# Kernel tuning notes

Measured on AMD Instinct MI355X. Metric: run time of the kernel, lower is better.

## Reference

```python
import jax, jax.numpy as jnp
import numpy as np

N = 10000      # nodes
E = 320000     # edges (before self-loops)
D_IN = 256
HID = 128
HEADS = 4
D_OUT = 256
SLOPE = 0.2    # PyG GATConv default negative_slope


def setup_inputs() -> dict:
    key = jax.random.key(0)
    ks = jax.random.split(key, 10)
    s = 0.05
    return {
        "x": jax.random.normal(ks[0], (N, D_IN), dtype=jnp.float32),
        "edge_index": jax.random.randint(ks[1], (2, E), 0, N),
        # layer 1: in=256 -> heads=4, out=128, concat
        "W1": jax.random.normal(ks[2], (D_IN, HEADS * HID), dtype=jnp.float32) * s,
        "a1_src": jax.random.normal(ks[3], (HEADS, HID), dtype=jnp.float32) * s,
        "a1_dst": jax.random.normal(ks[4], (HEADS, HID), dtype=jnp.float32) * s,
        "b1": jax.random.normal(ks[5], (HEADS * HID,), dtype=jnp.float32) * s,
        # layer 2: in=512 -> heads=1, out=256, no concat
        "W2": jax.random.normal(ks[6], (HEADS * HID, D_OUT), dtype=jnp.float32) * s,
        "a2_src": jax.random.normal(ks[7], (1, D_OUT), dtype=jnp.float32) * s,
        "a2_dst": jax.random.normal(ks[8], (1, D_OUT), dtype=jnp.float32) * s,
        "b2": jax.random.normal(ks[9], (D_OUT,), dtype=jnp.float32) * s,
    }


def gat_conv(x, src, dst, W, a_src, a_dst, bias, heads, out_dim, concat):
    """PyG-style GATConv (eval mode, self-loops pre-added to src/dst)."""
    n = x.shape[0]
    h = (x @ W).reshape(n, heads, out_dim)            # [N, H, F]
    # per-edge attention logits: LeakyReLU(a_src.h_src + a_dst.h_dst)
    as_n = (h * a_src).sum(-1)                         # [N, H]
    ad_n = (h * a_dst).sum(-1)                         # [N, H]
    logit = jax.nn.leaky_relu(as_n[src] + ad_n[dst], negative_slope=SLOPE)  # [E, H]
    # segment softmax over edges grouped by destination node
    logit = logit - jax.ops.segment_max(logit, dst, num_segments=n)[dst]
    ex = jnp.exp(logit)
    alpha = ex / jax.ops.segment_sum(ex, dst, num_segments=n)[dst]          # [E, H]
    # weighted scatter-aggregation of source messages
    out = jax.ops.segment_sum(h[src] * alpha[:, :, None], dst, num_segments=n)  # [N, H, F]
    out = out.reshape(n, heads * out_dim) if concat else out.mean(axis=1)
    return out + bias


def reference(x, edge_index, W1, a1_src, a1_dst, b1, W2, a2_src, a2_dst, b2):
    # add self-loops once (PyG GATConv default add_self_loops=True)
    loops = jnp.arange(N, dtype=edge_index.dtype)
    src = jnp.concatenate([edge_index[0], loops])
    dst = jnp.concatenate([edge_index[1], loops])
    h = gat_conv(x, src, dst, W1, a1_src, a1_dst, b1, HEADS, HID, True)
    h = jax.nn.elu(h)  # dropout is identity at eval
    return gat_conv(h, src, dst, W2, a2_src, a2_dst, b2, 1, D_OUT, False)
```

## Files before the change

kernel.cpp:

```cpp
#include <hip/hip_runtime.h>

#define N_NODES 10000
#define E_RAW   320000
#define E_TOT   330000
#define D_IN    256
#define HID     128
#define HEADS   4
#define F1      512
#define D_OUT   256
#define SLOPE   0.2f
#define EBLOCKS 1290

typedef __attribute__((ext_vector_type(8))) short bf16x8;
typedef __attribute__((ext_vector_type(4))) float f32x4;

__device__ __forceinline__ float bf2f(ushort u) {
    return __uint_as_float(((uint)u) << 16);
}
__device__ __forceinline__ ushort f2bf(float x) {
    uint u = __float_as_uint(x);
    uint r = (u + 0x7FFFu + ((u >> 16) & 1u)) >> 16;
    return (ushort)r;
}
__device__ __forceinline__ float bfu_lo(uint u) { return __uint_as_float(u << 16); }
__device__ __forceinline__ float bfu_hi(uint u) { return __uint_as_float(u & 0xFFFF0000u); }

__device__ __forceinline__ void gload_lds16(const void* g, void* l) {
    __builtin_amdgcn_global_load_lds(
        (const __attribute__((address_space(1))) void*)g,
        (__attribute__((address_space(3))) void*)l, 16, 0, 0);
}


__global__ __launch_bounds__(256) void k_zero_all(int* __restrict__ deg,
                                                  float* __restrict__ as1,
                                                  float* __restrict__ ad1,
                                                  float* __restrict__ as2,
                                                  float* __restrict__ ad2) {
    int i = blockIdx.x * 256 + threadIdx.x;
    if (i < 4 * N_NODES) { as1[i] = 0.f; ad1[i] = 0.f; }
    if (i < N_NODES) { deg[i] = 0; as2[i] = 0.f; ad2[i] = 0.f; }
}


__global__ __launch_bounds__(256) void k_hist(const int* __restrict__ ei, int* __restrict__ deg) {
    int e = blockIdx.x * 256 + threadIdx.x;
    if (e < E_TOT) {
        int dst = (e < E_RAW) ? ei[E_RAW + e] : (e - E_RAW);
        atomicAdd(&deg[dst], 1);
    }
}


#define SCAN_CHUNK 40

__global__ __launch_bounds__(256) void k_prep(const int* __restrict__ deg,
                                              int* __restrict__ row_start,
                                              int* __restrict__ cursor,
                                              const float* __restrict__ W1,
                                              ushort* __restrict__ w1h,
                                              const float* __restrict__ W2,
                                              ushort* __restrict__ w2h,
                                              const float* __restrict__ x,
                                              ushort* __restrict__ xb) {
    int b = blockIdx.x;
    int tid = threadIdx.x;
    if (b == 0) {
        __shared__ int tots[256];
        int base = tid * SCAN_CHUNK;
        int loc[SCAN_CHUNK];
        int s = 0;
        #pragma unroll
        for (int k = 0; k < SCAN_CHUNK; k++) {
            int idx = base + k;
            int v = (idx < N_NODES) ? deg[idx] : 0;
            loc[k] = s;
            s += v;
        }
        tots[tid] = s;
        __syncthreads();
        for (int off = 1; off < 256; off <<= 1) {
            int t = (tid >= off) ? tots[tid - off] : 0;
            __syncthreads();
            tots[tid] += t;
            __syncthreads();
        }
        int excl = tots[tid] - s;
        #pragma unroll
        for (int k = 0; k < SCAN_CHUNK; k++) {
            int idx = base + k;
            if (idx < N_NODES) {
                int r = excl + loc[k];
                row_start[idx] = r;
                cursor[idx]    = r;
            }
        }
        if (tid == 255) row_start[N_NODES] = E_TOT;
    } else if (b <= 64) {
        int task = (b - 1) * 4 + (tid >> 6);
        int lane = tid & 63;
        int n = (task >> 5) * 64 + lane;
        int k0 = (task & 31) * 8;
        float v[8];
        #pragma unroll
        for (int j = 0; j < 8; j++) v[j] = W1[(size_t)(k0 + j) * F1 + n];
        uint4 u;
        u.x = (uint)f2bf(v[0]) | ((uint)f2bf(v[1]) << 16);
        u.y = (uint)f2bf(v[2]) | ((uint)f2bf(v[3]) << 16);
        u.z = (uint)f2bf(v[4]) | ((uint)f2bf(v[5]) << 16);
        u.w = (uint)f2bf(v[6]) | ((uint)f2bf(v[7]) << 16);
        *(uint4*)&w1h[(size_t)n * D_IN + k0] = u;
    } else if (b <= 128) {
        int task = (b - 65) * 4 + (tid >> 6);
        int lane = tid & 63;
        int n = (task >> 6) * 64 + lane;
        int k0 = (task & 63) * 8;
        float v[8];
        #pragma unroll
        for (int j = 0; j < 8; j++) v[j] = W2[(size_t)(k0 + j) * D_OUT + n];
        uint4 u;
        u.x = (uint)f2bf(v[0]) | ((uint)f2bf(v[1]) << 16);
        u.y = (uint)f2bf(v[2]) | ((uint)f2bf(v[3]) << 16);
        u.z = (uint)f2bf(v[4]) | ((uint)f2bf(v[5]) << 16);
        u.w = (uint)f2bf(v[6]) | ((uint)f2bf(v[7]) << 16);
        *(uint4*)&w2h[(size_t)n * F1 + k0] = u;
    } else {
        int i8 = (b - 129) * 256 + tid;
        float4 a = *(const float4*)&x[(size_t)i8 * 8];
        float4 c = *(const float4*)&x[(size_t)i8 * 8 + 4];
        uint4 u;
        u.x = (uint)f2bf(a.x) | ((uint)f2bf(a.y) << 16);
        u.y = (uint)f2bf(a.z) | ((uint)f2bf(a.w) << 16);
        u.z = (uint)f2bf(c.x) | ((uint)f2bf(c.y) << 16);
        u.w = (uint)f2bf(c.z) | ((uint)f2bf(c.w) << 16);
        *(uint4*)&xb[(size_t)i8 * 8] = u;
    }
}


__global__ __launch_bounds__(256) void k_scatter(const int* __restrict__ ei,
                                                 int* __restrict__ cursor,
                                                 int* __restrict__ csr_src) {
    int e = blockIdx.x * 256 + threadIdx.x;
    if (e < E_TOT) {
        int src = (e < E_RAW) ? ei[e] : (e - E_RAW);
        int dst = (e < E_RAW) ? ei[E_RAW + e] : (e - E_RAW);
        int pos = atomicAdd(&cursor[dst], 1);
        csr_src[pos] = src;
    }
}


template<int BM, int KD, int ND, int WC, int HMUL>
__device__ __forceinline__ void gemm_attn(int bx, int by, int tid,
                                          const ushort* __restrict__ A,
                                          const ushort* __restrict__ B,
                                          ushort* __restrict__ C,
                                          const float* __restrict__ avs,
                                          const float* __restrict__ avd,
                                          float* __restrict__ os,
                                          float* __restrict__ od) {
    constexpr int WR = 4 / WC;
    constexpr int MI = (BM / WR) / 16;
    constexpr int NJ = (64 / WC) / 16;
    constexpr int NT = KD / 64;
    __shared__ ushort sA[2][BM * 64];
    __shared__ ushort sB[2][64 * 64];

    const int lane = tid & 63;
    const int wid = tid >> 6;
    const int wr = wid / WC;
    const int wc = wid % WC;
    const int m0 = by * BM;
    const int n0 = bx * 64;
    const int fr = lane & 15;
    const int fs = lane >> 4;
    const int rowc = lane >> 3;
    const int slot = (lane & 7) ^ rowc;

    f32x4 acc[MI][NJ];
    #pragma unroll
    for (int i = 0; i < MI; i++)
        #pragma unroll
        for (int j = 0; j < NJ; j++) acc[i][j] = (f32x4){0.f, 0.f, 0.f, 0.f};

    auto STAGE = [&](int buf, int k0) {
        #pragma unroll
        for (int t = 0; t < BM / 32; t++) {
            int c = wid + 4 * t;
            int gr = m0 + c * 8 + rowc;
            gr = gr < N_NODES ? gr : N_NODES - 1;
            gload_lds16(A + (size_t)gr * KD + k0 + slot * 8, &sA[buf][c * 512]);
        }
        #pragma unroll
        for (int t = 0; t < 2; t++) {
            int c = wid + 4 * t;
            gload_lds16(B + (size_t)(n0 + c * 8 + rowc) * KD + k0 + slot * 8, &sB[buf][c * 512]);
        }
    };
    auto COMPUTE = [&](int buf) {
        #pragma unroll
        for (int kk = 0; kk < 2; kk++) {
            int sbase = kk * 4 + fs;
            bf16x8 a_f[MI], b_f[NJ];
            #pragma unroll
            for (int i = 0; i < MI; i++) {
                int r = wr * 64 + i * 16 + fr;
                a_f[i] = *(const bf16x8*)&sA[buf][r * 64 + ((sbase ^ (r & 7)) << 3)];
            }
            #pragma unroll
            for (int j = 0; j < NJ; j++) {
                int cc = wc * (64 / WC) + j * 16 + fr;
                b_f[j] = *(const bf16x8*)&sB[buf][cc * 64 + ((sbase ^ (cc & 7)) << 3)];
            }
            #pragma unroll
            for (int i = 0; i < MI; i++)
                #pragma unroll
                for (int j = 0; j < NJ; j++)
                    acc[i][j] = __builtin_amdgcn_mfma_f32_16x16x32_bf16(a_f[i], b_f[j], acc[i][j], 0, 0, 0);
        }
    };

    STAGE(0, 0);
    __syncthreads();
    int cur = 0;
    #pragma unroll
    for (int t = 0; t < NT - 1; t++) {
        STAGE(cur ^ 1, (t + 1) * 64);
        COMPUTE(cur);
        __syncthreads();
        cur ^= 1;
    }
    COMPUTE(cur);

    const int hoff = (HMUL == 4) ? (n0 >> 7) : 0;
    float sv[NJ], dv[NJ];
    int cols[NJ];
    #pragma unroll
    for (int j = 0; j < NJ; j++) {
        cols[j] = n0 + wc * (64 / WC) + j * 16 + fr;
        sv[j] = avs[cols[j]];
        dv[j] = avd[cols[j]];
    }
    #pragma unroll
    for (int i = 0; i < MI; i++) {
        int row_base = m0 + wr * 64 + i * 16 + (fs << 2);
        float ps[4], pd[4];
        #pragma unroll
        for (int q = 0; q < 4; q++) {
            int r = row_base + q;
            float p_s = 0.f, p_d = 0.f;
            #pragma unroll
            for (int j = 0; j < NJ; j++) {
                float v = acc[i][j][q];
                if (r < N_NODES) C[(size_t)r * ND + cols[j]] = f2bf(v);
                p_s += v * sv[j];
                p_d += v * dv[j];
            }
            ps[q] = p_s; pd[q] = p_d;
        }
        #pragma unroll
        for (int q = 0; q < 4; q++) {
            #pragma unroll
            for (int m = 8; m >= 1; m >>= 1) {
                ps[q] += __shfl_xor(ps[q], m, 16);
                pd[q] += __shfl_xor(pd[q], m, 16);
            }
        }
        if (fr == 0) {
            #pragma unroll
            for (int q = 0; q < 4; q++) {
                int r = row_base + q;
                if (r < N_NODES) {
                    atomicAdd(&os[r * HMUL + hoff], ps[q]);
                    atomicAdd(&od[r * HMUL + hoff], pd[q]);
                }
            }
        }
    }
}


__global__ __launch_bounds__(256) void k_gemm1(const ushort* __restrict__ xb,
                                               const ushort* __restrict__ w1h,
                                               ushort* __restrict__ h1,
                                               const float* __restrict__ a1s,
                                               const float* __restrict__ a1d,
                                               float* __restrict__ as1,
                                               float* __restrict__ ad1) {
    int g = blockIdx.x;
    gemm_attn<128, D_IN, F1, 2, 4>(g % 8, g / 8, threadIdx.x,
                                   xb, w1h, h1, a1s, a1d, as1, ad1);
}


__global__ __launch_bounds__(256) void k_gemm2(const ushort* __restrict__ heluh,
                                               const ushort* __restrict__ w2h,
                                               ushort* __restrict__ h2,
                                               const float* __restrict__ a2s,
                                               const float* __restrict__ a2d,
                                               float* __restrict__ as2,
                                               float* __restrict__ ad2) {
    int b = blockIdx.x;
    gemm_attn<64, F1, D_OUT, 4, 1>(b % 4, b / 4, threadIdx.x,
                                   heluh, w2h, h2, a2s, a2d, as2, ad2);
}


__device__ __forceinline__ void fma8(uint4 v, float e, float* acc) {
    acc[0] += bfu_lo(v.x) * e; acc[1] += bfu_hi(v.x) * e;
    acc[2] += bfu_lo(v.y) * e; acc[3] += bfu_hi(v.y) * e;
    acc[4] += bfu_lo(v.z) * e; acc[5] += bfu_hi(v.z) * e;
    acc[6] += bfu_lo(v.w) * e; acc[7] += bfu_hi(v.w) * e;
}

__global__ __launch_bounds__(256) void k_edge1(const int* __restrict__ row_start,
                                               const int* __restrict__ csr_src,
                                               const ushort* __restrict__ h1,
                                               const float* __restrict__ as1,
                                               const float* __restrict__ ad1,
                                               const float* __restrict__ b1,
                                               ushort* __restrict__ heluh) {
    int node = blockIdx.x * 4 + (threadIdx.x >> 6);
    int lane = threadIdx.x & 63;
    int start = row_start[node];
    int end   = row_start[node + 1];
    int h_lane = lane >> 4;

    float adl = ad1[node * 4 + h_lane];

    float acc[8] = {0,0,0,0,0,0,0,0};
    float sum = 0.f;
    const size_t lo8 = (size_t)lane * 8;

    int i = start;
    for (; i + 8 <= end; i += 8) {
        int s[8];
        #pragma unroll
        for (int k = 0; k < 8; k++) s[k] = csr_src[i + k];
        float l[8];
        #pragma unroll
        for (int k = 0; k < 8; k++) l[k] = as1[s[k] * 4 + h_lane];
        uint4 v[8];
        #pragma unroll
        for (int k = 0; k < 8; k++) v[k] = *(const uint4*)(h1 + (size_t)s[k] * F1 + lo8);
        #pragma unroll
        for (int k = 0; k < 8; k++) {
            float t = l[k] + adl;
            t = t > 0.f ? t : SLOPE * t;
            float e = __expf(t);
            sum += e;
            fma8(v[k], e, acc);
        }
    }
    for (; i < end; i++) {
        int s0 = csr_src[i];
        float t = as1[s0 * 4 + h_lane] + adl;
        uint4 v0 = *(const uint4*)(h1 + (size_t)s0 * F1 + lo8);
        t = t > 0.f ? t : SLOPE * t;
        float e = __expf(t);
        sum += e;
        fma8(v0, e, acc);
    }
    float inv = 1.f / sum;

    size_t o = (size_t)node * F1 + lo8;
    const float* bp = b1 + lo8;
    uint pk[4];
    #pragma unroll
    for (int j = 0; j < 4; j++) {
        float v0 = acc[2*j]   * inv + bp[2*j];
        float v1 = acc[2*j+1] * inv + bp[2*j+1];
        v0 = v0 > 0.f ? v0 : (__expf(v0) - 1.f);
        v1 = v1 > 0.f ? v1 : (__expf(v1) - 1.f);
        pk[j] = (uint)f2bf(v0) | ((uint)f2bf(v1) << 16);
    }
    *(uint4*)&heluh[o] = make_uint4(pk[0], pk[1], pk[2], pk[3]);
}

__global__ __launch_bounds__(256) void k_edge2(const int* __restrict__ row_start,
                                               const int* __restrict__ csr_src,
                                               const ushort* __restrict__ h2,
                                               const float* __restrict__ as2,
                                               const float* __restrict__ ad2,
                                               const float* __restrict__ b2,
                                               float* __restrict__ out) {
    int node = blockIdx.x * 4 + (threadIdx.x >> 6);
    int lane = threadIdx.x & 63;
    int sub = lane >> 5;
    int fl  = lane & 31;
    int start = row_start[node];
    int end   = row_start[node + 1];

    float ad = ad2[node];

    float acc[8] = {0,0,0,0,0,0,0,0};
    float sum = 0.f;
    const size_t fo = (size_t)fl * 8;

    int i = start;
    for (; i + 8 <= end; i += 8) {
        int s[4];
        #pragma unroll
        for (int k = 0; k < 4; k++) s[k] = csr_src[i + 2 * k + sub];
        float l[4];
        #pragma unroll
        for (int k = 0; k < 4; k++) l[k] = as2[s[k]];
        uint4 v[4];
        #pragma unroll
        for (int k = 0; k < 4; k++) v[k] = *(const uint4*)(h2 + (size_t)s[k] * D_OUT + fo);
        #pragma unroll
        for (int k = 0; k < 4; k++) {
            float t = l[k] + ad;
            t = t > 0.f ? t : SLOPE * t;
            float e = __expf(t);
            sum += e;
            fma8(v[k], e, acc);
        }
    }
    for (; i < end; i += 2) {
        if (i + sub < end) {
            int s0 = csr_src[i + sub];
            float t = as2[s0] + ad;
            uint4 v0 = *(const uint4*)(h2 + (size_t)s0 * D_OUT + fo);
            t = t > 0.f ? t : SLOPE * t;
            float e = __expf(t);
            sum += e;
            fma8(v0, e, acc);
        }
    }
    #pragma unroll
    for (int j = 0; j < 8; j++) acc[j] += __shfl_xor(acc[j], 32, 64);
    sum += __shfl_xor(sum, 32, 64);
    float inv = 1.f / sum;

    if (lane < 32) {
        size_t o = (size_t)node * D_OUT + fo;
        const float* bp = b2 + fo;
        float4 r0, r1;
        r0.x = acc[0] * inv + bp[0]; r0.y = acc[1] * inv + bp[1];
        r0.z = acc[2] * inv + bp[2]; r0.w = acc[3] * inv + bp[3];
        r1.x = acc[4] * inv + bp[4]; r1.y = acc[5] * inv + bp[5];
        r1.z = acc[6] * inv + bp[6]; r1.w = acc[7] * inv + bp[7];
        *(float4*)&out[o] = r0;
        *(float4*)&out[o + 4] = r1;
    }
}


extern "C" void kernel_launch(void* const* d_in, const int* in_sizes, int n_in,
                              void* d_out, int out_size, void* d_ws, size_t ws_size,
                              hipStream_t stream) {
    const float* x   = (const float*)d_in[0];
    const int*   ei  = (const int*)d_in[1];
    const float* W1  = (const float*)d_in[2];
    const float* a1s = (const float*)d_in[3];
    const float* a1d = (const float*)d_in[4];
    const float* b1  = (const float*)d_in[5];
    const float* W2  = (const float*)d_in[6];
    const float* a2s = (const float*)d_in[7];
    const float* a2d = (const float*)d_in[8];
    const float* b2  = (const float*)d_in[9];
    float* out = (float*)d_out;

    char* ws = (char*)d_ws;
    size_t off = 0;
    auto take = [&](size_t bytes) {
        char* p = ws + off;
        off += (bytes + 255) & ~(size_t)255;
        return p;
    };
    int*    deg       = (int*)take(sizeof(int) * N_NODES);
    int*    row_start = (int*)take(sizeof(int) * (N_NODES + 1));
    int*    cursor    = (int*)take(sizeof(int) * N_NODES);
    int*    csr_src   = (int*)take(sizeof(int) * E_TOT);
    ushort* xb        = (ushort*)take(sizeof(ushort) * (size_t)N_NODES * D_IN);
    ushort* w1h       = (ushort*)take(sizeof(ushort) * D_IN * F1);
    ushort* w2h       = (ushort*)take(sizeof(ushort) * F1 * D_OUT);
    ushort* h1        = (ushort*)take(sizeof(ushort) * (size_t)N_NODES * F1);
    float*  as1       = (float*)take(sizeof(float) * N_NODES * 4);
    float*  ad1       = (float*)take(sizeof(float) * N_NODES * 4);
    ushort* heluh     = (ushort*)take(sizeof(ushort) * (size_t)N_NODES * F1);
    ushort* h2        = (ushort*)take(sizeof(ushort) * (size_t)N_NODES * D_OUT);
    float*  as2       = (float*)take(sizeof(float) * N_NODES);
    float*  ad2       = (float*)take(sizeof(float) * N_NODES);

    k_zero_all<<<(4 * N_NODES + 255) / 256, 256, 0, stream>>>(deg, as1, ad1, as2, ad2);
    k_hist<<<EBLOCKS, 256, 0, stream>>>(ei, deg);
    k_prep<<<1379, 256, 0, stream>>>(deg, row_start, cursor, W1, w1h, W2, w2h, x, xb);
    k_scatter<<<EBLOCKS, 256, 0, stream>>>(ei, cursor, csr_src);
    k_gemm1<<<8 * 79, 256, 0, stream>>>(xb, w1h, h1, a1s, a1d, as1, ad1);
    k_edge1<<<N_NODES / 4, 256, 0, stream>>>(row_start, csr_src, h1, as1, ad1, b1, heluh);
    k_gemm2<<<4 * 157, 256, 0, stream>>>(heluh, w2h, h2, a2s, a2d, as2, ad2);
    k_edge2<<<N_NODES / 4, 256, 0, stream>>>(row_start, csr_src, h2, as2, ad2, b2, out);
}
```

Before: 175.7 us.

## Fuse all GAT stages into one persistent cooperative kernel with grid syncs

Replaces the eight separate kernel launches with a single cooperative persistent kernel that walks through the stages as grid-stride job loops separated by grid.sync(). The CSR build now records a per-edge rank from the histogram atomic and places each edge with row_start+rank, so the cursor-based atomic scatter is no longer needed. The scan is overlapped with the first GEMM. Both GEMMs shrink to 64x64 tiles with a single LDS buffer, so the double-buffered prefetch is gone. The aim is to cut launch gaps and tail effects, at the cost of grid-wide barrier overhead, a grid capped at 1024 blocks, and possibly lower GEMM efficiency.

```diff
diff --git a/kernel.cpp b/kernel.cpp
--- a/kernel.cpp
+++ b/kernel.cpp
@@ -1,15 +1,27 @@
 #include <hip/hip_runtime.h>
+#include <hip/hip_cooperative_groups.h>
+
+namespace cg = cooperative_groups;
 
 #define N_NODES 10000
 #define E_RAW   320000
 #define E_TOT   330000
 #define D_IN    256
 #define HID     128
-#define HEADS   4
 #define F1      512
 #define D_OUT   256
 #define SLOPE   0.2f
-#define EBLOCKS 1290
+#define SCAN_CHUNK 40
+
+#define P0_ZERO 157
+#define P0_XB   1250
+#define P0_W1   64
+#define P0_W2   64
+#define P0_TOT  (P0_ZERO + P0_XB + P0_W1 + P0_W2)
+#define PE_TOT  1290
+#define G1_TILES 1256
+#define G2_TILES 628
+#define EDGE_JOBS 2500
 
 typedef __attribute__((ext_vector_type(8))) short bf16x8;
 typedef __attribute__((ext_vector_type(4))) float f32x4;
@@ -31,233 +43,182 @@
         (__attribute__((address_space(3))) void*)l, 16, 0, 0);
 }
 
-
-__global__ __launch_bounds__(256) void k_zero_all(int* __restrict__ deg,
-                                                  float* __restrict__ as1,
-                                                  float* __restrict__ ad1,
-                                                  float* __restrict__ as2,
-                                                  float* __restrict__ ad2) {
-    int i = blockIdx.x * 256 + threadIdx.x;
-    if (i < 4 * N_NODES) { as1[i] = 0.f; ad1[i] = 0.f; }
-    if (i < N_NODES) { deg[i] = 0; as2[i] = 0.f; ad2[i] = 0.f; }
-}
-
-
-__global__ __launch_bounds__(256) void k_hist(const int* __restrict__ ei, int* __restrict__ deg) {
-    int e = blockIdx.x * 256 + threadIdx.x;
-    if (e < E_TOT) {
-        int dst = (e < E_RAW) ? ei[E_RAW + e] : (e - E_RAW);
-        atomicAdd(&deg[dst], 1);
-    }
-}
-
-
-#define SCAN_CHUNK 40
-
-__global__ __launch_bounds__(256) void k_prep(const int* __restrict__ deg,
-                                              int* __restrict__ row_start,
-                                              int* __restrict__ cursor,
-                                              const float* __restrict__ W1,
-                                              ushort* __restrict__ w1h,
-                                              const float* __restrict__ W2,
-                                              ushort* __restrict__ w2h,
-                                              const float* __restrict__ x,
-                                              ushort* __restrict__ xb) {
-    int b = blockIdx.x;
-    int tid = threadIdx.x;
-    if (b == 0) {
-        __shared__ int tots[256];
-        int base = tid * SCAN_CHUNK;
-        int loc[SCAN_CHUNK];
-        int s = 0;
-        #pragma unroll
-        for (int k = 0; k < SCAN_CHUNK; k++) {
-            int idx = base + k;
-            int v = (idx < N_NODES) ? deg[idx] : 0;
-            loc[k] = s;
-            s += v;
-        }
-        tots[tid] = s;
-        __syncthreads();
-        for (int off = 1; off < 256; off <<= 1) {
-            int t = (tid >= off) ? tots[tid - off] : 0;
-            __syncthreads();
-            tots[tid] += t;
-            __syncthreads();
-        }
-        int excl = tots[tid] - s;
-        #pragma unroll
-        for (int k = 0; k < SCAN_CHUNK; k++) {
-            int idx = base + k;
-            if (idx < N_NODES) {
-                int r = excl + loc[k];
-                row_start[idx] = r;
-                cursor[idx]    = r;
-            }
-        }
-        if (tid == 255) row_start[N_NODES] = E_TOT;
-    } else if (b <= 64) {
-        int task = (b - 1) * 4 + (tid >> 6);
+struct Args {
+    const float* x;
+    const int*   ei;
+    const float* W1;
+    const float* a1s;
+    const float* a1d;
+    const float* b1;
+    const float* W2;
+    const float* a2s;
+    const float* a2d;
+    const float* b2;
+    float*       out;
+    int*         deg;
+    int*         rank;
+    int*         row_start;
+    int*         csr_src;
+    ushort*      xb;
+    ushort*      w1h;
+    ushort*      w2h;
+    ushort*      h1;
+    float*       as1;
+    float*       ad1;
+    ushort*      heluh;
+    ushort*      h2;
+    float*       as2;
+    float*       ad2;
+};
+
+
+__device__ __forceinline__ void p0_job(const Args& a, int j, int tid) {
+    if (j < P0_ZERO) {
+        int i = j * 256 + tid;
+        if (i < 4 * N_NODES) { a.as1[i] = 0.f; a.ad1[i] = 0.f; }
+        if (i < N_NODES) { a.deg[i] = 0; a.as2[i] = 0.f; a.ad2[i] = 0.f; }
+    } else if (j < P0_ZERO + P0_XB) {
+        int i8 = (j - P0_ZERO) * 256 + tid;
+        float4 v0 = *(const float4*)&a.x[(size_t)i8 * 8];
+        float4 v1 = *(const float4*)&a.x[(size_t)i8 * 8 + 4];
+        uint4 u;
+        u.x = (uint)f2bf(v0.x) | ((uint)f2bf(v0.y) << 16);
+        u.y = (uint)f2bf(v0.z) | ((uint)f2bf(v0.w) << 16);
+        u.z = (uint)f2bf(v1.x) | ((uint)f2bf(v1.y) << 16);
+        u.w = (uint)f2bf(v1.z) | ((uint)f2bf(v1.w) << 16);
+        *(uint4*)&a.xb[(size_t)i8 * 8] = u;
+    } else if (j < P0_ZERO + P0_XB + P0_W1) {
+        int task = (j - (P0_ZERO + P0_XB)) * 4 + (tid >> 6);
         int lane = tid & 63;
         int n = (task >> 5) * 64 + lane;
         int k0 = (task & 31) * 8;
         float v[8];
         #pragma unroll
-        for (int j = 0; j < 8; j++) v[j] = W1[(size_t)(k0 + j) * F1 + n];
+        for (int q = 0; q < 8; q++) v[q] = a.W1[(size_t)(k0 + q) * F1 + n];
         uint4 u;
         u.x = (uint)f2bf(v[0]) | ((uint)f2bf(v[1]) << 16);
         u.y = (uint)f2bf(v[2]) | ((uint)f2bf(v[3]) << 16);
         u.z = (uint)f2bf(v[4]) | ((uint)f2bf(v[5]) << 16);
         u.w = (uint)f2bf(v[6]) | ((uint)f2bf(v[7]) << 16);
-        *(uint4*)&w1h[(size_t)n * D_IN + k0] = u;
-    } else if (b <= 128) {
-        int task = (b - 65) * 4 + (tid >> 6);
+        *(uint4*)&a.w1h[(size_t)n * D_IN + k0] = u;
+    } else {
+        int task = (j - (P0_ZERO + P0_XB + P0_W1)) * 4 + (tid >> 6);
         int lane = tid & 63;
         int n = (task >> 6) * 64 + lane;
         int k0 = (task & 63) * 8;
         float v[8];
         #pragma unroll
-        for (int j = 0; j < 8; j++) v[j] = W2[(size_t)(k0 + j) * D_OUT + n];
+        for (int q = 0; q < 8; q++) v[q] = a.W2[(size_t)(k0 + q) * D_OUT + n];
         uint4 u;
         u.x = (uint)f2bf(v[0]) | ((uint)f2bf(v[1]) << 16);
         u.y = (uint)f2bf(v[2]) | ((uint)f2bf(v[3]) << 16);
         u.z = (uint)f2bf(v[4]) | ((uint)f2bf(v[5]) << 16);
         u.w = (uint)f2bf(v[6]) | ((uint)f2bf(v[7]) << 16);
-        *(uint4*)&w2h[(size_t)n * F1 + k0] = u;
-    } else {
-        int i8 = (b - 129) * 256 + tid;
-        float4 a = *(const float4*)&x[(size_t)i8 * 8];
-        float4 c = *(const float4*)&x[(size_t)i8 * 8 + 4];
-        uint4 u;
-        u.x = (uint)f2bf(a.x) | ((uint)f2bf(a.y) << 16);
-        u.y = (uint)f2bf(a.z) | ((uint)f2bf(a.w) << 16);
-        u.z = (uint)f2bf(c.x) | ((uint)f2bf(c.y) << 16);
-        u.w = (uint)f2bf(c.z) | ((uint)f2bf(c.w) << 16);
-        *(uint4*)&xb[(size_t)i8 * 8] = u;
-    }
-}
-
-
-__global__ __launch_bounds__(256) void k_scatter(const int* __restrict__ ei,
-                                                 int* __restrict__ cursor,
-                                                 int* __restrict__ csr_src) {
-    int e = blockIdx.x * 256 + threadIdx.x;
-    if (e < E_TOT) {
-        int src = (e < E_RAW) ? ei[e] : (e - E_RAW);
-        int dst = (e < E_RAW) ? ei[E_RAW + e] : (e - E_RAW);
-        int pos = atomicAdd(&cursor[dst], 1);
-        csr_src[pos] = src;
-    }
-}
-
-
-template<int BM, int KD, int ND, int WC, int HMUL>
-__device__ __forceinline__ void gemm_attn(int bx, int by, int tid,
-                                          const ushort* __restrict__ A,
-                                          const ushort* __restrict__ B,
-                                          ushort* __restrict__ C,
-                                          const float* __restrict__ avs,
-                                          const float* __restrict__ avd,
-                                          float* __restrict__ os,
-                                          float* __restrict__ od) {
-    constexpr int WR = 4 / WC;
-    constexpr int MI = (BM / WR) / 16;
-    constexpr int NJ = (64 / WC) / 16;
-    constexpr int NT = KD / 64;
-    __shared__ ushort sA[2][BM * 64];
-    __shared__ ushort sB[2][64 * 64];
-
+        *(uint4*)&a.w2h[(size_t)n * F1 + k0] = u;
+    }
+}
+
+
+__device__ __forceinline__ void scan_job(const Args& a, int tid, int* tots) {
+    int base = tid * SCAN_CHUNK;
+    int loc[SCAN_CHUNK];
+    int s = 0;
+    #pragma unroll
+    for (int k = 0; k < SCAN_CHUNK; k++) {
+        int idx = base + k;
+        int v = (idx < N_NODES) ? a.deg[idx] : 0;
+        loc[k] = s;
+        s += v;
+    }
+    tots[tid] = s;
+    __syncthreads();
+    for (int off = 1; off < 256; off <<= 1) {
+        int t = (tid >= off) ? tots[tid - off] : 0;
+        __syncthreads();
+        tots[tid] += t;
+        __syncthreads();
+    }
+    int excl = tots[tid] - s;
+    #pragma unroll
+    for (int k = 0; k < SCAN_CHUNK; k++) {
+        int idx = base + k;
+        if (idx < N_NODES) a.row_start[idx] = excl + loc[k];
+    }
+    if (tid == 255) a.row_start[N_NODES] = E_TOT;
+    __syncthreads();
+}
+
+
+template<int KD, int ND, int HMUL>
+__device__ __forceinline__ void gemm_job(int job, int tid, ushort* sA, ushort* sB,
+                                         const ushort* __restrict__ A,
+                                         const ushort* __restrict__ B,
+                                         ushort* __restrict__ C,
+                                         const float* __restrict__ avs,
+                                         const float* __restrict__ avd,
+                                         float* __restrict__ os,
+                                         float* __restrict__ od) {
+    constexpr int TX = ND / 64;
+    const int bx = job % TX;
+    const int by = job / TX;
     const int lane = tid & 63;
     const int wid = tid >> 6;
-    const int wr = wid / WC;
-    const int wc = wid % WC;
-    const int m0 = by * BM;
+    const int m0 = by * 64;
     const int n0 = bx * 64;
     const int fr = lane & 15;
     const int fs = lane >> 4;
     const int rowc = lane >> 3;
     const int slot = (lane & 7) ^ rowc;
 
-    f32x4 acc[MI][NJ];
-    #pragma unroll
-    for (int i = 0; i < MI; i++)
-        #pragma unroll
-        for (int j = 0; j < NJ; j++) acc[i][j] = (f32x4){0.f, 0.f, 0.f, 0.f};
-
-    auto STAGE = [&](int buf, int k0) {
-        #pragma unroll
-        for (int t = 0; t < BM / 32; t++) {
+    f32x4 acc[4];
+    #pragma unroll
+    for (int i = 0; i < 4; i++) acc[i] = (f32x4){0.f, 0.f, 0.f, 0.f};
+
+    for (int k0 = 0; k0 < KD; k0 += 64) {
+        #pragma unroll
+        for (int t = 0; t < 2; t++) {
             int c = wid + 4 * t;
             int gr = m0 + c * 8 + rowc;
             gr = gr < N_NODES ? gr : N_NODES - 1;
-            gload_lds16(A + (size_t)gr * KD + k0 + slot * 8, &sA[buf][c * 512]);
+            gload_lds16(A + (size_t)gr * KD + k0 + slot * 8, &sA[c * 512]);
         }
         #pragma unroll
         for (int t = 0; t < 2; t++) {
             int c = wid + 4 * t;
-            gload_lds16(B + (size_t)(n0 + c * 8 + rowc) * KD + k0 + slot * 8, &sB[buf][c * 512]);
-        }
-    };
-    auto COMPUTE = [&](int buf) {
+            gload_lds16(B + (size_t)(n0 + c * 8 + rowc) * KD + k0 + slot * 8, &sB[c * 512]);
+        }
+        __syncthreads();
         #pragma unroll
         for (int kk = 0; kk < 2; kk++) {
             int sbase = kk * 4 + fs;
-            bf16x8 a_f[MI], b_f[NJ];
+            bf16x8 af[4], bf;
             #pragma unroll
-            for (int i = 0; i < MI; i++) {
-                int r = wr * 64 + i * 16 + fr;
-                a_f[i] = *(const bf16x8*)&sA[buf][r * 64 + ((sbase ^ (r & 7)) << 3)];
+            for (int i = 0; i < 4; i++) {
+                int r = i * 16 + fr;
+                af[i] = *(const bf16x8*)&sA[r * 64 + ((sbase ^ (r & 7)) << 3)];
             }
+            int cc = wid * 16 + fr;
+            bf = *(const bf16x8*)&sB[cc * 64 + ((sbase ^ (cc & 7)) << 3)];
             #pragma unroll
-            for (int j = 0; j < NJ; j++) {
-                int cc = wc * (64 / WC) + j * 16 + fr;
-                b_f[j] = *(const bf16x8*)&sB[buf][cc * 64 + ((sbase ^ (cc & 7)) << 3)];
-            }
-            #pragma unroll
-            for (int i = 0; i < MI; i++)
-                #pragma unroll
-                for (int j = 0; j < NJ; j++)
-                    acc[i][j] = __builtin_amdgcn_mfma_f32_16x16x32_bf16(a_f[i], b_f[j], acc[i][j], 0, 0, 0);
-        }
-    };
-
-    STAGE(0, 0);
-    __syncthreads();
-    int cur = 0;
-    #pragma unroll
-    for (int t = 0; t < NT - 1; t++) {
-        STAGE(cur ^ 1, (t + 1) * 64);
-        COMPUTE(cur);
+            for (int i = 0; i < 4; i++)
+                acc[i] = __builtin_amdgcn_mfma_f32_16x16x32_bf16(af[i], bf, acc[i], 0, 0, 0);
+        }
         __syncthreads();
-        cur ^= 1;
-    }
-    COMPUTE(cur);
+    }
 
     const int hoff = (HMUL == 4) ? (n0 >> 7) : 0;
-    float sv[NJ], dv[NJ];
-    int cols[NJ];
-    #pragma unroll
-    for (int j = 0; j < NJ; j++) {
-        cols[j] = n0 + wc * (64 / WC) + j * 16 + fr;
-        sv[j] = avs[cols[j]];
-        dv[j] = avd[cols[j]];
-    }
-    #pragma unroll
-    for (int i = 0; i < MI; i++) {
-        int row_base = m0 + wr * 64 + i * 16 + (fs << 2);
+    const int col = n0 + wid * 16 + fr;
+    const float sv = avs[col], dv = avd[col];
+    #pragma unroll
+    for (int i = 0; i < 4; i++) {
+        int row_base = m0 + i * 16 + (fs << 2);
         float ps[4], pd[4];
         #pragma unroll
         for (int q = 0; q < 4; q++) {
+            float v = acc[i][q];
             int r = row_base + q;
-            float p_s = 0.f, p_d = 0.f;
-            #pragma unroll
-            for (int j = 0; j < NJ; j++) {
-                float v = acc[i][j][q];
-                if (r < N_NODES) C[(size_t)r * ND + cols[j]] = f2bf(v);
-                p_s += v * sv[j];
-                p_d += v * dv[j];
-            }
-            ps[q] = p_s; pd[q] = p_d;
+            if (r < N_NODES) C[(size_t)r * ND + col] = f2bf(v);
+            ps[q] = v * sv; pd[q] = v * dv;
         }
         #pragma unroll
         for (int q = 0; q < 4; q++) {
@@ -281,32 +242,6 @@
 }
 
 
-__global__ __launch_bounds__(256) void k_gemm1(const ushort* __restrict__ xb,
-                                               const ushort* __restrict__ w1h,
-                                               ushort* __restrict__ h1,
-                                               const float* __restrict__ a1s,
-                                               const float* __restrict__ a1d,
-                                               float* __restrict__ as1,
-                                               float* __restrict__ ad1) {
-    int g = blockIdx.x;
-    gemm_attn<128, D_IN, F1, 2, 4>(g % 8, g / 8, threadIdx.x,
-                                   xb, w1h, h1, a1s, a1d, as1, ad1);
-}
-
-
-__global__ __launch_bounds__(256) void k_gemm2(const ushort* __restrict__ heluh,
-                                               const ushort* __restrict__ w2h,
-                                               ushort* __restrict__ h2,
-                                               const float* __restrict__ a2s,
-                                               const float* __restrict__ a2d,
-                                               float* __restrict__ as2,
-                                               float* __restrict__ ad2) {
-    int b = blockIdx.x;
-    gemm_attn<64, F1, D_OUT, 4, 1>(b % 4, b / 4, threadIdx.x,
-                                   heluh, w2h, h2, a2s, a2d, as2, ad2);
-}
-
-
 __device__ __forceinline__ void fma8(uint4 v, float e, float* acc) {
     acc[0] += bfu_lo(v.x) * e; acc[1] += bfu_hi(v.x) * e;
     acc[2] += bfu_lo(v.y) * e; acc[3] += bfu_hi(v.y) * e;
@@ -314,21 +249,14 @@
     acc[6] += bfu_lo(v.w) * e; acc[7] += bfu_hi(v.w) * e;
 }
 
-__global__ __launch_bounds__(256) void k_edge1(const int* __restrict__ row_start,
-                                               const int* __restrict__ csr_src,
-                                               const ushort* __restrict__ h1,
-                                               const float* __restrict__ as1,
-                                               const float* __restrict__ ad1,
-                                               const float* __restrict__ b1,
-                                               ushort* __restrict__ heluh) {
-    int node = blockIdx.x * 4 + (threadIdx.x >> 6);
-    int lane = threadIdx.x & 63;
-    int start = row_start[node];
-    int end   = row_start[node + 1];
+__device__ __forceinline__ void edge1_job(const Args& a, int job, int tid) {
+    int node = job * 4 + (tid >> 6);
+    int lane = tid & 63;
+    int start = a.row_start[node];
+    int end   = a.row_start[node + 1];
     int h_lane = lane >> 4;
 
-    float adl = ad1[node * 4 + h_lane];
-
+    float adl = a.ad1[node * 4 + h_lane];
     float acc[8] = {0,0,0,0,0,0,0,0};
     float sum = 0.f;
     const size_t lo8 = (size_t)lane * 8;
@@ -337,13 +265,13 @@
     for (; i + 8 <= end; i += 8) {
         int s[8];
         #pragma unroll
-        for (int k = 0; k < 8; k++) s[k] = csr_src[i + k];
+        for (int k = 0; k < 8; k++) s[k] = a.csr_src[i + k];
         float l[8];
         #pragma unroll
-        for (int k = 0; k < 8; k++) l[k] = as1[s[k] * 4 + h_lane];
+        for (int k = 0; k < 8; k++) l[k] = a.as1[s[k] * 4 + h_lane];
         uint4 v[8];
         #pragma unroll
-        for (int k = 0; k < 8; k++) v[k] = *(const uint4*)(h1 + (size_t)s[k] * F1 + lo8);
+        for (int k = 0; k < 8; k++) v[k] = *(const uint4*)(a.h1 + (size_t)s[k] * F1 + lo8);
         #pragma unroll
         for (int k = 0; k < 8; k++) {
             float t = l[k] + adl;
@@ -354,9 +282,9 @@
         }
     }
     for (; i < end; i++) {
-        int s0 = csr_src[i];
-        float t = as1[s0 * 4 + h_lane] + adl;
-        uint4 v0 = *(const uint4*)(h1 + (size_t)s0 * F1 + lo8);
+        int s0 = a.csr_src[i];
+        float t = a.as1[s0 * 4 + h_lane] + adl;
+        uint4 v0 = *(const uint4*)(a.h1 + (size_t)s0 * F1 + lo8);
         t = t > 0.f ? t : SLOPE * t;
         float e = __expf(t);
         sum += e;
@@ -365,7 +293,7 @@
     float inv = 1.f / sum;
 
     size_t o = (size_t)node * F1 + lo8;
-    const float* bp = b1 + lo8;
+    const float* bp = a.b1 + lo8;
     uint pk[4];
     #pragma unroll
     for (int j = 0; j < 4; j++) {
@@ -375,25 +303,18 @@
         v1 = v1 > 0.f ? v1 : (__expf(v1) - 1.f);
         pk[j] = (uint)f2bf(v0) | ((uint)f2bf(v1) << 16);
     }
-    *(uint4*)&heluh[o] = make_uint4(pk[0], pk[1], pk[2], pk[3]);
-}
-
-__global__ __launch_bounds__(256) void k_edge2(const int* __restrict__ row_start,
-                                               const int* __restrict__ csr_src,
-                                               const ushort* __restrict__ h2,
-                                               const float* __restrict__ as2,
-                                               const float* __restrict__ ad2,
-                                               const float* __restrict__ b2,
-                                               float* __restrict__ out) {
-    int node = blockIdx.x * 4 + (threadIdx.x >> 6);
-    int lane = threadIdx.x & 63;
+    *(uint4*)&a.heluh[o] = make_uint4(pk[0], pk[1], pk[2], pk[3]);
+}
+
+__device__ __forceinline__ void edge2_job(const Args& a, int job, int tid) {
+    int node = job * 4 + (tid >> 6);
+    int lane = tid & 63;
     int sub = lane >> 5;
     int fl  = lane & 31;
-    int start = row_start[node];
-    int end   = row_start[node + 1];
-
-    float ad = ad2[node];
-
+    int start = a.row_start[node];
+    int end   = a.row_start[node + 1];
+
+    float ad = a.ad2[node];
     float acc[8] = {0,0,0,0,0,0,0,0};
     float sum = 0.f;
     const size_t fo = (size_t)fl * 8;
@@ -402,13 +323,13 @@
     for (; i + 8 <= end; i += 8) {
         int s[4];
         #pragma unroll
-        for (int k = 0; k < 4; k++) s[k] = csr_src[i + 2 * k + sub];
+        for (int k = 0; k < 4; k++) s[k] = a.csr_src[i + 2 * k + sub];
         float l[4];
         #pragma unroll
-        for (int k = 0; k < 4; k++) l[k] = as2[s[k]];
+        for (int k = 0; k < 4; k++) l[k] = a.as2[s[k]];
         uint4 v[4];
         #pragma unroll
-        for (int k = 0; k < 4; k++) v[k] = *(const uint4*)(h2 + (size_t)s[k] * D_OUT + fo);
+        for (int k = 0; k < 4; k++) v[k] = *(const uint4*)(a.h2 + (size_t)s[k] * D_OUT + fo);
         #pragma unroll
         for (int k = 0; k < 4; k++) {
             float t = l[k] + ad;
@@ -420,9 +341,9 @@
     }
     for (; i < end; i += 2) {
         if (i + sub < end) {
-            int s0 = csr_src[i + sub];
-            float t = as2[s0] + ad;
-            uint4 v0 = *(const uint4*)(h2 + (size_t)s0 * D_OUT + fo);
+            int s0 = a.csr_src[i + sub];
+            float t = a.as2[s0] + ad;
+            uint4 v0 = *(const uint4*)(a.h2 + (size_t)s0 * D_OUT + fo);
             t = t > 0.f ? t : SLOPE * t;
             float e = __expf(t);
             sum += e;
@@ -436,33 +357,70 @@
 
     if (lane < 32) {
         size_t o = (size_t)node * D_OUT + fo;
-        const float* bp = b2 + fo;
+        const float* bp = a.b2 + fo;
         float4 r0, r1;
         r0.x = acc[0] * inv + bp[0]; r0.y = acc[1] * inv + bp[1];
         r0.z = acc[2] * inv + bp[2]; r0.w = acc[3] * inv + bp[3];
         r1.x = acc[4] * inv + bp[4]; r1.y = acc[5] * inv + bp[5];
         r1.z = acc[6] * inv + bp[6]; r1.w = acc[7] * inv + bp[7];
-        *(float4*)&out[o] = r0;
-        *(float4*)&out[o + 4] = r1;
-    }
+        *(float4*)&a.out[o] = r0;
+        *(float4*)&a.out[o + 4] = r1;
+    }
+}
+
+
+__global__ __launch_bounds__(256, 4) void k_mega(Args a) {
+    cg::grid_group grid = cg::this_grid();
+    __shared__ ushort smem[8192];
+    ushort* sA = smem;
+    ushort* sB = smem + 4096;
+    const int tid = threadIdx.x;
+    const int nb = gridDim.x;
+
+    for (int j = blockIdx.x; j < P0_TOT; j += nb) p0_job(a, j, tid);
+    grid.sync();
+
+    for (int j = blockIdx.x; j < PE_TOT; j += nb) {
+        int e = j * 256 + tid;
+        if (e < E_TOT) {
+            int dst = (e < E_RAW) ? a.ei[E_RAW + e] : (e - E_RAW);
+            a.rank[e] = atomicAdd(&a.deg[dst], 1);
+        }
+    }
+    grid.sync();
+
+    for (int j = blockIdx.x; j < 1 + G1_TILES; j += nb) {
+        if (j == 0) scan_job(a, tid, (int*)smem);
+        else gemm_job<D_IN, F1, 4>(j - 1, tid, sA, sB, a.xb, a.w1h, a.h1,
+                                   a.a1s, a.a1d, a.as1, a.ad1);
+    }
+    grid.sync();
+
+    for (int j = blockIdx.x; j < PE_TOT; j += nb) {
+        int e = j * 256 + tid;
+        if (e < E_TOT) {
+            int src = (e < E_RAW) ? a.ei[e] : (e - E_RAW);
+            int dst = (e < E_RAW) ? a.ei[E_RAW + e] : (e - E_RAW);
+            a.csr_src[a.row_start[dst] + a.rank[e]] = src;
+        }
+    }
+    grid.sync();
+
+    for (int j = blockIdx.x; j < EDGE_JOBS; j += nb) edge1_job(a, j, tid);
+    grid.sync();
+
+    for (int j = blockIdx.x; j < G2_TILES; j += nb)
+        gemm_job<F1, D_OUT, 1>(j, tid, sA, sB, a.heluh, a.w2h, a.h2,
+                               a.a2s, a.a2d, a.as2, a.ad2);
+    grid.sync();
+
+    for (int j = blockIdx.x; j < EDGE_JOBS; j += nb) edge2_job(a, j, tid);
 }
 
 
 extern "C" void kernel_launch(void* const* d_in, const int* in_sizes, int n_in,
                               void* d_out, int out_size, void* d_ws, size_t ws_size,
                               hipStream_t stream) {
-    const float* x   = (const float*)d_in[0];
-    const int*   ei  = (const int*)d_in[1];
-    const float* W1  = (const float*)d_in[2];
-    const float* a1s = (const float*)d_in[3];
-    const float* a1d = (const float*)d_in[4];
-    const float* b1  = (const float*)d_in[5];
-    const float* W2  = (const float*)d_in[6];
-    const float* a2s = (const float*)d_in[7];
-    const float* a2d = (const float*)d_in[8];
-    const float* b2  = (const float*)d_in[9];
-    float* out = (float*)d_out;
-
     char* ws = (char*)d_ws;
     size_t off = 0;
     auto take = [&](size_t bytes) {
@@ -470,27 +428,41 @@
         off += (bytes + 255) & ~(size_t)255;
         return p;
     };
-    int*    deg       = (int*)take(sizeof(int) * N_NODES);
-    int*    row_start = (int*)take(sizeof(int) * (N_NODES + 1));
-    int*    cursor    = (int*)take(sizeof(int) * N_NODES);
-    int*    csr_src   = (int*)take(sizeof(int) * E_TOT);
-    ushort* xb        = (ushort*)take(sizeof(ushort) * (size_t)N_NODES * D_IN);
-    ushort* w1h       = (ushort*)take(sizeof(ushort) * D_IN * F1);
-    ushort* w2h       = (ushort*)take(sizeof(ushort) * F1 * D_OUT);
-    ushort* h1        = (ushort*)take(sizeof(ushort) * (size_t)N_NODES * F1);
-    float*  as1       = (float*)take(sizeof(float) * N_NODES * 4);
-    float*  ad1       = (float*)take(sizeof(float) * N_NODES * 4);
-    ushort* heluh     = (ushort*)take(sizeof(ushort) * (size_t)N_NODES * F1);
-    ushort* h2        = (ushort*)take(sizeof(ushort) * (size_t)N_NODES * D_OUT);
-    float*  as2       = (float*)take(sizeof(float) * N_NODES);
-    float*  ad2       = (float*)take(sizeof(float) * N_NODES);
-
-    k_zero_all<<<(4 * N_NODES + 255) / 256, 256, 0, stream>>>(deg, as1, ad1, as2, ad2);
-    k_hist<<<EBLOCKS, 256, 0, stream>>>(ei, deg);
-    k_prep<<<1379, 256, 0, stream>>>(deg, row_start, cursor, W1, w1h, W2, w2h, x, xb);
-    k_scatter<<<EBLOCKS, 256, 0, stream>>>(ei, cursor, csr_src);
-    k_gemm1<<<8 * 79, 256, 0, stream>>>(xb, w1h, h1, a1s, a1d, as1, ad1);
-    k_edge1<<<N_NODES / 4, 256, 0, stream>>>(row_start, csr_src, h1, as1, ad1, b1, heluh);
-    k_gemm2<<<4 * 157, 256, 0, stream>>>(heluh, w2h, h2, a2s, a2d, as2, ad2);
-    k_edge2<<<N_NODES / 4, 256, 0, stream>>>(row_start, csr_src, h2, as2, ad2, b2, out);
-}
+
+    Args a;
+    a.x   = (const float*)d_in[0];
+    a.ei  = (const int*)d_in[1];
+    a.W1  = (const float*)d_in[2];
+    a.a1s = (const float*)d_in[3];
+    a.a1d = (const float*)d_in[4];
+    a.b1  = (const float*)d_in[5];
+    a.W2  = (const float*)d_in[6];
+    a.a2s = (const float*)d_in[7];
+    a.a2d = (const float*)d_in[8];
+    a.b2  = (const float*)d_in[9];
+    a.out = (float*)d_out;
+
+    a.deg       = (int*)take(sizeof(int) * N_NODES);
+    a.rank      = (int*)take(sizeof(int) * E_TOT);
+    a.row_start = (int*)take(sizeof(int) * (N_NODES + 1));
+    a.csr_src   = (int*)take(sizeof(int) * E_TOT);
+    a.xb        = (ushort*)take(sizeof(ushort) * (size_t)N_NODES * D_IN);
+    a.w1h       = (ushort*)take(sizeof(ushort) * D_IN * F1);
+    a.w2h       = (ushort*)take(sizeof(ushort) * F1 * D_OUT);
+    a.h1        = (ushort*)take(sizeof(ushort) * (size_t)N_NODES * F1);
+    a.as1       = (float*)take(sizeof(float) * N_NODES * 4);
+    a.ad1       = (float*)take(sizeof(float) * N_NODES * 4);
+    a.heluh     = (ushort*)take(sizeof(ushort) * (size_t)N_NODES * F1);
+    a.h2        = (ushort*)take(sizeof(ushort) * (size_t)N_NODES * D_OUT);
+    a.as2       = (float*)take(sizeof(float) * N_NODES);
+    a.ad2       = (float*)take(sizeof(float) * N_NODES);
+
+    int maxb = 0;
+    hipError_t err = hipOccupancyMaxActiveBlocksPerMultiprocessor(&maxb, (const void*)k_mega, 256, 0);
+    if (err != hipSuccess || maxb <= 0) maxb = 3;
+    int grid = maxb * 256;
+    if (grid > 1024) grid = 1024;
+
+    void* params[] = { &a };
+    hipLaunchCooperativeKernel((const void*)k_mega, dim3(grid), dim3(256), params, 0, stream);
+}
```

Result: slower. 547.7 us (+211.8%).
